# Performance work log

Hardware: AMD Instinct MI355X
Metric: run time of the kernel (lower is better)

Reference implementation:

```python
import jax, jax.numpy as jnp
import numpy as np

N_NODES = 50000
N_EDGES = 262144
N_OCP = 32768
N_GRAPHS = 64
H = 128          # hidden_size
F_IN = 128       # node feature dim (== H for the stub GNN)
N_LABELS = 10


def _lin(key, fan_in, fan_out):
    return jax.random.normal(key, (fan_in, fan_out), jnp.float32) * (1.0 / float(np.sqrt(fan_in)))


def setup_inputs() -> dict:
    key = jax.random.key(0)
    ks = jax.random.split(key, 16)
    x = jax.random.normal(ks[0], (N_NODES, F_IN), jnp.float32)
    edge_index = jax.random.randint(ks[1], (2, N_EDGES), 0, N_NODES)
    batch_vec = jnp.sort(jax.random.randint(ks[2], (N_NODES,), 0, N_GRAPHS))
    y = jax.random.randint(ks[3], (N_GRAPHS,), 0, N_LABELS)
    params = {
        # stub GNN (get_node_reps): one GCN-style layer
        'W_self': _lin(ks[4], F_IN, H),
        'W_nbr': _lin(ks[5], F_IN, H),
        'b_gnn': jnp.zeros((H,), jnp.float32),
        # edge_action_rep_generator: Linear(2H,4H) ELU Linear(4H,2H) ELU Linear(2H,H)
        'Wr1': _lin(ks[6], 2 * H, 4 * H), 'br1': jnp.zeros((4 * H,), jnp.float32),
        'Wr2': _lin(ks[7], 4 * H, 2 * H), 'br2': jnp.zeros((2 * H,), jnp.float32),
        'Wr3': _lin(ks[8], 2 * H, H),     'br3': jnp.zeros((H,), jnp.float32),
        # edge_action_prob_generator: Linear(H,H) ELU Linear(H,num_labels)
        'Wp1': _lin(ks[9], H, H),         'bp1': jnp.zeros((H,), jnp.float32),
        'Wp2': _lin(ks[10], H, N_LABELS), 'bp2': jnp.zeros((N_LABELS,), jnp.float32),
    }
    return dict(x=x, edge_index=edge_index, batch_vec=batch_vec, y=y, n_ocp=N_OCP, **params)


def reference(x, edge_index, batch_vec, y, n_ocp,
              W_self, W_nbr, b_gnn,
              Wr1, br1, Wr2, br2, Wr3, br3,
              Wp1, bp1, Wp2, bp2):
    N = x.shape[0]
    G = y.shape[0]

    def get_node_reps(ei):
        # stub for self.model.get_node_reps: elu(x @ W_self + A @ (x @ W_nbr))
        msg = x[ei[0]] @ W_nbr                                   # [E', H]
        agg = jax.ops.segment_sum(msg, ei[1], num_segments=N)    # [N, H]
        return jax.nn.elu(x @ W_self + agg + b_gnn)

    ocp_edge_index = edge_index[:, :n_ocp]    # state == True edges
    ava_edge_index = edge_index[:, n_ocp:]    # state == False edges

    ava_node_reps = get_node_reps(edge_index) - get_node_reps(ocp_edge_index)  # [N, H]

    # gather per available edge + concat src/dst reps -> [E_ava, 2H]
    a = jnp.concatenate([ava_node_reps[ava_edge_index[0]],
                         ava_node_reps[ava_edge_index[1]]], axis=1)
    # edge_action_rep_generator
    a = jax.nn.elu(a @ Wr1 + br1)
    a = jax.nn.elu(a @ Wr2 + br2)
    a = a @ Wr3 + br3                                            # [E_ava, H]
    # edge_action_prob_generator
    h = jax.nn.elu(a @ Wp1 + bp1)
    logits = h @ Wp2 + bp2                                       # [E_ava, L]

    seg = batch_vec[ava_edge_index[0]]                           # graph id per ava edge
    y_edge = y[seg]                                              # target label per edge
    sel = jnp.take_along_axis(logits, y_edge[:, None], axis=1)[:, 0]  # gather(1, y)

    # segment-wise softmax over edges of each graph
    mx = jax.ops.segment_max(sel, seg, num_segments=G)
    ex = jnp.exp(sel - mx[seg])
    probs = ex / jax.ops.segment_sum(ex, seg, num_segments=G)[seg]    # [E_ava]

    # scatter_max: per-graph max prob and its argmax edge index
    pmax = jax.ops.segment_max(probs, seg, num_segments=G)            # [G]
    E = probs.shape[0]
    idx = jnp.where(probs == pmax[seg], jnp.arange(E), E)
    added_actions = jax.ops.segment_min(idx, seg, num_segments=G)     # [G]

    return probs, pmax, added_actions
```

## Files before the change

kernel.cpp:

```cpp
#include <hip/hip_runtime.h>

#define NN   50000
#define NNP  50048
#define NE   262144
#define NOCP 32768
#define EAVA (NE - NOCP)
#define NG   64
#define HD   128
#define CAP  48
#define CHNK 32768

typedef _Float16 f16x8 __attribute__((ext_vector_type(8)));
typedef _Float16 f16x2 __attribute__((ext_vector_type(2)));
typedef float f32x4 __attribute__((ext_vector_type(4)));

#define WAITVM12() asm volatile("s_waitcnt vmcnt(12)" ::: "memory")
#define WAITVM6()  asm volatile("s_waitcnt vmcnt(6)" ::: "memory")
#define WAITVM0()  asm volatile("s_waitcnt vmcnt(0)" ::: "memory")

__device__ __forceinline__ float elu_f(float v) { return v > 0.f ? v : (expf(v) - 1.f); }

__device__ __forceinline__ unsigned fenc(float f) {
  unsigned u = __float_as_uint(f);
  return (u & 0x80000000u) ? ~u : (u | 0x80000000u);
}
__device__ __forceinline__ float fdec(unsigned u) {
  return __uint_as_float((u & 0x80000000u) ? (u & 0x7fffffffu) : ~u);
}

__device__ __forceinline__ void dma16(const void* g, void* l) {
  __builtin_amdgcn_global_load_lds((const __attribute__((address_space(1))) unsigned int*)g,
                                   (__attribute__((address_space(3))) unsigned int*)l,
                                   16, 0, 0);
}

__global__ __launch_bounds__(256) void zero_i(int* __restrict__ p, int n) {
  for (int i = blockIdx.x * 256 + threadIdx.x; i < n; i += gridDim.x * 256) p[i] = 0;
}

__global__ void init_small(unsigned* mx_enc, float* denom, unsigned* pmax_enc, int* amin) {
  int t = threadIdx.x;
  if (t < NG) { mx_enc[t] = 0u; denom[t] = 0.f; pmax_enc[t] = 0u; amin[t] = EAVA; }
}

__global__ __launch_bounds__(256) void zero_tails(_Float16* __restrict__ base) {
  int t = blockIdx.x * 256 + threadIdx.x;
  if (t >= 6 * 768) return;
  int arr = t / 768, off = t % 768;
  f16x8 z = {};
  *(f16x8*)(base + (size_t)arr * NNP * HD + (size_t)NN * HD + (size_t)off * 8) = z;
}

__global__ __launch_bounds__(256) void bucket_kernel(const int* __restrict__ ei,
    int* __restrict__ cnt, int* __restrict__ bucket) {
  int e = blockIdx.x * 256 + threadIdx.x;
  if (e >= NE) return;
  int dst = ei[NE + e];
  int src = ei[e];
  int slot = atomicAdd(&cnt[dst], 1);
  if (slot < CAP)
    bucket[(size_t)dst * CAP + slot] = (int)((unsigned)src | (e < NOCP ? 0x80000000u : 0u));
}

__global__ __launch_bounds__(256) void gather_kernel(const float* __restrict__ x,
    const int* __restrict__ cnt, const int* __restrict__ bucket,
    _Float16* __restrict__ xsah, _Float16* __restrict__ xsal,
    _Float16* __restrict__ xsoh, _Float16* __restrict__ xsol) {
  int n = blockIdx.x * 4 + (threadIdx.x >> 6);
  if (n >= NN) return;
  int lane = threadIdx.x & 63;
  int c = cnt[n];
  if (c > CAP) c = CAP;
  float2 aall = make_float2(0.f, 0.f), aocp = aall;
  const int* bk = bucket + (size_t)n * CAP;
  for (int i0 = 0; i0 < c; i0 += 4) {
    int4 pk = *(const int4*)(bk + i0);
    bool m1 = (i0 + 1 < c), m2 = (i0 + 2 < c), m3 = (i0 + 3 < c);
    int r0 = pk.x & 0x7fffffff;
    int r1 = m1 ? (pk.y & 0x7fffffff) : 0;
    int r2 = m2 ? (pk.z & 0x7fffffff) : 0;
    int r3 = m3 ? (pk.w & 0x7fffffff) : 0;
    float2 v0 = *(const float2*)(x + (size_t)r0 * HD + lane * 2);
    float2 v1 = *(const float2*)(x + (size_t)r1 * HD + lane * 2);
    float2 v2 = *(const float2*)(x + (size_t)r2 * HD + lane * 2);
    float2 v3 = *(const float2*)(x + (size_t)r3 * HD + lane * 2);
    aall.x += v0.x; aall.y += v0.y;
    if (pk.x < 0) { aocp.x += v0.x; aocp.y += v0.y; }
    if (m1) { aall.x += v1.x; aall.y += v1.y; if (pk.y < 0) { aocp.x += v1.x; aocp.y += v1.y; } }
    if (m2) { aall.x += v2.x; aall.y += v2.y; if (pk.z < 0) { aocp.x += v2.x; aocp.y += v2.y; } }
    if (m3) { aall.x += v3.x; aall.y += v3.y; if (pk.w < 0) { aocp.x += v3.x; aocp.y += v3.y; } }
  }
  size_t o = (size_t)n * HD + lane * 2;
  _Float16 h0 = (_Float16)aall.x, h1 = (_Float16)aall.y;
  *(f16x2*)(xsah + o) = (f16x2){h0, h1};
  *(f16x2*)(xsal + o) = (f16x2){(_Float16)(aall.x - (float)h0), (_Float16)(aall.y - (float)h1)};
  _Float16 g0 = (_Float16)aocp.x, g1 = (_Float16)aocp.y;
  *(f16x2*)(xsoh + o) = (f16x2){g0, g1};
  *(f16x2*)(xsol + o) = (f16x2){(_Float16)(aocp.x - (float)g0), (_Float16)(aocp.y - (float)g1)};
}

__global__ __launch_bounds__(256) void split_x(const float* __restrict__ r,
    _Float16* __restrict__ rh, _Float16* __restrict__ rl) {
  int t = blockIdx.x * 256 + threadIdx.x;
  if (t >= NN * HD / 8) return;
  const float4* p = (const float4*)(r + (size_t)t * 8);
  float4 v0 = p[0], v1 = p[1];
  float vv[8] = {v0.x, v0.y, v0.z, v0.w, v1.x, v1.y, v1.z, v1.w};
  f16x8 hv, lv;
#pragma unroll
  for (int j = 0; j < 8; ++j) {
    _Float16 hh = (_Float16)vv[j];
    hv[j] = hh;
    lv[j] = (_Float16)(vv[j] - (float)hh);
  }
  *(f16x8*)(rh + (size_t)t * 8) = hv;
  *(f16x8*)(rl + (size_t)t * 8) = lv;
}

__global__ void pack_w2(const float* __restrict__ Wself, const float* __restrict__ Wnbr,
    _Float16* __restrict__ oh, _Float16* __restrict__ ol) {
  int chunk = blockIdx.x;
  int lane = threadIdx.x;
  int ns = chunk & 7, kt = chunk >> 3;
  int n = ns * 16 + (lane & 15);
  int k0 = kt * 32 + (lane >> 4) * 8;
  f16x8 hv, lv;
#pragma unroll
  for (int j = 0; j < 8; ++j) {
    int k = k0 + j;
    float v = (k < 128) ? Wself[(size_t)k * 128 + n] : Wnbr[(size_t)(k - 128) * 128 + n];
    _Float16 hh = (_Float16)v;
    hv[j] = hh;
    lv[j] = (_Float16)(v - (float)hh);
  }
  *(f16x8*)(oh + (size_t)chunk * 512 + lane * 8) = hv;
  *(f16x8*)(ol + (size_t)chunk * 512 + lane * 8) = lv;
}

__global__ void pack_w(const float* __restrict__ W, int K, int N,
    _Float16* __restrict__ oh, _Float16* __restrict__ ol) {
  int chunk = blockIdx.x;
  int lane = threadIdx.x;
  int NS = N >> 4;
  int ns = chunk % NS, kt = chunk / NS;
  int n = ns * 16 + (lane & 15);
  int k0 = kt * 32 + (lane >> 4) * 8;
  f16x8 hv, lv;
#pragma unroll
  for (int j = 0; j < 8; ++j) {
    float v = W[(size_t)(k0 + j) * N + n];
    _Float16 hh = (_Float16)v;
    hv[j] = hh;
    lv[j] = (_Float16)(v - (float)hh);
  }
  *(f16x8*)(oh + (size_t)chunk * 512 + lane * 8) = hv;
  *(f16x8*)(ol + (size_t)chunk * 512 + lane * 8) = lv;
}

__global__ void w34_kernel(const float* __restrict__ Wr3, const float* __restrict__ Wp1,
    const float* __restrict__ br3, const float* __restrict__ bp1,
    float* __restrict__ W34, float* __restrict__ b34) {
  int i = blockIdx.x, j = threadIdx.x;
  float s = 0.f;
  for (int k = 0; k < 128; ++k) s += Wr3[i * 128 + k] * Wp1[k * 128 + j];
  W34[i * 128 + j] = s;
  if (i == 0) {
    float t = bp1[j];
    for (int k = 0; k < 128; ++k) t += br3[k] * Wp1[k * 128 + j];
    b34[j] = t;
  }
}

template <int KT, int NS_B, int AMODE, int KT_NEXT, int NB>
__global__ __launch_bounds__(256) void gemm_ab(
    const _Float16* __restrict__ Ah, const _Float16* __restrict__ Al,
    const int* __restrict__ idx0, const int* __restrict__ idx1,
    const _Float16* __restrict__ Bh, const _Float16* __restrict__ Bl,
    const float* __restrict__ bias,
    _Float16* __restrict__ Oh, _Float16* __restrict__ Ol) {
  __shared__ char smem[73728] __attribute__((aligned(16)));
  float* sC = (float*)smem;

  const int tid = threadIdx.x;
  const int w = tid >> 6, lane = tid & 63;
  const int l16 = lane & 15, g16 = lane >> 4;
  const int f = blockIdx.x;
  const int r8 = f & 7;
  const int nb = (f >> 3) % NB;
  const int q8 = f / (8 * NB);
  const int bm = (q8 * 8 + r8) * 128, bn = nb * 64;
  const int w2r = w >> 1, w2c = w & 1;
  const int bmT = bm >> 4, bnS = bn >> 4;

  f32x4 acc[4][2];
#pragma unroll
  for (int i = 0; i < 4; ++i)
#pragma unroll
    for (int j = 0; j < 2; ++j) acc[i][j] = (f32x4)0.f;

  int i0a = 0, i0b = 0, i1a = 0, i1b = 0;
  if constexpr (AMODE == 1) {
    int rr0 = bm + w * 32 + l16;
    i0a = idx0[rr0]; i0b = idx0[rr0 + 16];
    i1a = idx1[rr0]; i1b = idx1[rr0 + 16];
  }

  auto STAGE = [&](int kt, int buf) {
    char* base = smem + buf * 24576;
    if constexpr (AMODE == 0) {
#pragma unroll
      for (int s = 0; s < 2; ++s) {
        int msub = w * 2 + s;
        size_t ch = (size_t)(bmT + msub) * KT + kt;
        dma16((const char*)Ah + ch * 1024 + lane * 16, base + msub * 1024);
        dma16((const char*)Al + ch * 1024 + lane * 16, base + 8192 + msub * 1024);
      }
    } else {
      int col = (kt & 3) * 32 + g16 * 8;
      int r0 = (kt < 4) ? i0a : i1a;
      int r1 = (kt < 4) ? i0b : i1b;
      dma16(Ah + (size_t)r0 * HD + col, base + (w * 2) * 1024);
      dma16(Al + (size_t)r0 * HD + col, base + 8192 + (w * 2) * 1024);
      dma16(Ah + (size_t)r1 * HD + col, base + (w * 2 + 1) * 1024);
      dma16(Al + (size_t)r1 * HD + col, base + 8192 + (w * 2 + 1) * 1024);
    }
    size_t chb = (size_t)kt * NS_B + bnS + w;
    dma16((const char*)Bh + chb * 1024 + lane * 16, base + 16384 + w * 1024);
    dma16((const char*)Bl + chb * 1024 + lane * 16, base + 20480 + w * 1024);
  };

  auto COMPUTE = [&](int buf) {
    const _Float16* sAh = (const _Float16*)(smem + buf * 24576);
    const _Float16* sAl = (const _Float16*)(smem + buf * 24576 + 8192);
    const _Float16* sBh = (const _Float16*)(smem + buf * 24576 + 16384);
    const _Float16* sBl = (const _Float16*)(smem + buf * 24576 + 20480);
    f16x8 ah[4], al[4];
#pragma unroll
    for (int mi = 0; mi < 4; ++mi) {
      ah[mi] = *(const f16x8*)(sAh + (w2r * 4 + mi) * 512 + lane * 8);
      al[mi] = *(const f16x8*)(sAl + (w2r * 4 + mi) * 512 + lane * 8);
    }
#pragma unroll
    for (int ni = 0; ni < 2; ++ni) {
      f16x8 bh = *(const f16x8*)(sBh + (w2c * 2 + ni) * 512 + lane * 8);
      f16x8 bl = *(const f16x8*)(sBl + (w2c * 2 + ni) * 512 + lane * 8);
#pragma unroll
      for (int mi = 0; mi < 4; ++mi) {
        acc[mi][ni] = __builtin_amdgcn_mfma_f32_16x16x32_f16(ah[mi], bh, acc[mi][ni], 0, 0, 0);
        acc[mi][ni] = __builtin_amdgcn_mfma_f32_16x16x32_f16(al[mi], bh, acc[mi][ni], 0, 0, 0);
        acc[mi][ni] = __builtin_amdgcn_mfma_f32_16x16x32_f16(ah[mi], bl, acc[mi][ni], 0, 0, 0);
      }
    }
  };

  STAGE(0, 0);
  STAGE(1, 1);
#pragma unroll
  for (int kt = 0; kt < KT; ++kt) {
    if (kt + 2 < KT) STAGE(kt + 2, (kt + 2) % 3);
    if (kt < KT - 2) WAITVM12();
    else if (kt == KT - 2) WAITVM6();
    else WAITVM0();
    __builtin_amdgcn_s_barrier();
    COMPUTE(kt % 3);
    __builtin_amdgcn_s_barrier();
  }

#pragma unroll
  for (int ni = 0; ni < 2; ++ni) {
    int colL = (w2c * 2 + ni) * 16 + l16;
    float bv = bias[bn + colL];
#pragma unroll
    for (int mi = 0; mi < 4; ++mi) {
      int rowb = w2r * 64 + mi * 16 + g16 * 4;
#pragma unroll
      for (int r = 0; r < 4; ++r)
        sC[(rowb + r) * 68 + colL] = elu_f(acc[mi][ni][r] + bv);
    }
  }
  __syncthreads();
  const int bnT32 = bn >> 5;
#pragma unroll
  for (int c = 0; c < 4; ++c) {
    int chunkid = w * 4 + c;
    int msub = chunkid >> 1, ktl = chunkid & 1;
    int m = msub * 16 + l16;
    int cb = ktl * 32 + g16 * 8;
    f16x8 hv, lv;
#pragma unroll
    for (int j = 0; j < 8; ++j) {
      float v = sC[m * 68 + cb + j];
      _Float16 hh = (_Float16)v;
      hv[j] = hh;
      lv[j] = (_Float16)(v - (float)hh);
    }
    size_t gchunk = (size_t)(bmT + msub) * KT_NEXT + (bnT32 + ktl);
    *(f16x8*)((char*)Oh + gchunk * 1024 + lane * 16) = hv;
    *(f16x8*)((char*)Ol + gchunk * 1024 + lane * 16) = lv;
  }
}

__global__ __launch_bounds__(64) void reps_direct(
    const _Float16* __restrict__ xh, const _Float16* __restrict__ xl,
    const _Float16* __restrict__ xsah, const _Float16* __restrict__ xsal,
    const _Float16* __restrict__ xsoh, const _Float16* __restrict__ xsol,
    const _Float16* __restrict__ Wsh, const _Float16* __restrict__ Wsl,
    const float* __restrict__ bias,
    _Float16* __restrict__ Oh, _Float16* __restrict__ Ol) {
  __shared__ float sC[32][68];
  const int lane = threadIdx.x;
  const int mt = blockIdx.x, nt = blockIdx.y;
  const int bm = mt * 32, bn = nt * 64;
  const int l16 = lane & 15, g16 = lane >> 4;

  f32x4 acc1[2][4], acc2[2][4];
#pragma unroll
  for (int i = 0; i < 2; ++i)
#pragma unroll
    for (int j = 0; j < 4; ++j) acc1[i][j] = (f32x4)0.f;

  auto CP3 = [&](f32x4 (*acc)[4], const f16x8* ah, const f16x8* al,
                 const f16x8* bh, const f16x8* bl) {
#pragma unroll
    for (int ni = 0; ni < 4; ++ni)
#pragma unroll
      for (int mi = 0; mi < 2; ++mi) {
        acc[mi][ni] = __builtin_amdgcn_mfma_f32_16x16x32_f16(ah[mi], bh[ni], acc[mi][ni], 0, 0, 0);
        acc[mi][ni] = __builtin_amdgcn_mfma_f32_16x16x32_f16(al[mi], bh[ni], acc[mi][ni], 0, 0, 0);
        acc[mi][ni] = __builtin_amdgcn_mfma_f32_16x16x32_f16(ah[mi], bl[ni], acc[mi][ni], 0, 0, 0);
      }
  };

#pragma unroll
  for (int kt = 0; kt < 4; ++kt) {
    f16x8 ah[2], al[2], bh[4], bl[4];
#pragma unroll
    for (int mi = 0; mi < 2; ++mi) {
      size_t off = (size_t)(bm + mi * 16 + l16) * HD + kt * 32 + g16 * 8;
      ah[mi] = *(const f16x8*)(xh + off);
      al[mi] = *(const f16x8*)(xl + off);
    }
#pragma unroll
    for (int ni = 0; ni < 4; ++ni) {
      size_t ch = (size_t)kt * 8 + nt * 4 + ni;
      bh[ni] = *(const f16x8*)(Wsh + ch * 512 + lane * 8);
      bl[ni] = *(const f16x8*)(Wsl + ch * 512 + lane * 8);
    }
    CP3(acc1, ah, al, bh, bl);
  }
#pragma unroll
  for (int i = 0; i < 2; ++i)
#pragma unroll
    for (int j = 0; j < 4; ++j) acc2[i][j] = acc1[i][j];

#pragma unroll
  for (int kt = 0; kt < 4; ++kt) {
    f16x8 aah[2], aal[2], aoh[2], aol[2], bh[4], bl[4];
#pragma unroll
    for (int mi = 0; mi < 2; ++mi) {
      size_t off = (size_t)(bm + mi * 16 + l16) * HD + kt * 32 + g16 * 8;
      aah[mi] = *(const f16x8*)(xsah + off);
      aal[mi] = *(const f16x8*)(xsal + off);
      aoh[mi] = *(const f16x8*)(xsoh + off);
      aol[mi] = *(const f16x8*)(xsol + off);
    }
#pragma unroll
    for (int ni = 0; ni < 4; ++ni) {
      size_t ch = (size_t)(kt + 4) * 8 + nt * 4 + ni;
      bh[ni] = *(const f16x8*)(Wsh + ch * 512 + lane * 8);
      bl[ni] = *(const f16x8*)(Wsl + ch * 512 + lane * 8);
    }
    CP3(acc1, aah, aal, bh, bl);
    CP3(acc2, aoh, aol, bh, bl);
  }

#pragma unroll
  for (int ni = 0; ni < 4; ++ni) {
    int colL = ni * 16 + l16;
    float bv = bias[bn + colL];
#pragma unroll
    for (int mi = 0; mi < 2; ++mi) {
      int rowb = mi * 16 + g16 * 4;
#pragma unroll
      for (int r = 0; r < 4; ++r)
        sC[rowb + r][colL] = elu_f(acc1[mi][ni][r] + bv) - elu_f(acc2[mi][ni][r] + bv);
    }
  }
  __syncthreads();
#pragma unroll
  for (int c = 0; c < 4; ++c) {
    int msub = c >> 1, ktl = c & 1;
    int m = msub * 16 + l16;
    int cb = ktl * 32 + g16 * 8;
    int grow = bm + m;
    if (grow < NN) {
      f16x8 hv, lv;
#pragma unroll
      for (int j = 0; j < 8; ++j) {
        float v = sC[m][cb + j];
        _Float16 hh = (_Float16)v;
        hv[j] = hh;
        lv[j] = (_Float16)(v - (float)hh);
      }
      *(f16x8*)(Oh + (size_t)grow * HD + bn + cb) = hv;
      *(f16x8*)(Ol + (size_t)grow * HD + bn + cb) = lv;
    }
  }
}

__global__ __launch_bounds__(256) void gemm3_sel(
    const _Float16* __restrict__ Ah, const _Float16* __restrict__ Al,
    const _Float16* __restrict__ Bh, const _Float16* __restrict__ Bl,
    const float* __restrict__ b34,
    const int* __restrict__ ei, const int* __restrict__ batchv, const int* __restrict__ yv,
    const float* __restrict__ Wp2, const float* __restrict__ bp2,
    float* __restrict__ sel, int* __restrict__ seg, int co) {
  __shared__ char smem[73728] __attribute__((aligned(16)));
  const int tid = threadIdx.x;
  const int w = tid >> 6, lane = tid & 63;
  const int l16 = lane & 15, g16 = lane >> 4;
  const int mt = blockIdx.x;

  f32x4 acc[8];
#pragma unroll
  for (int j = 0; j < 8; ++j) acc[j] = (f32x4)0.f;

  auto STAGE = [&](int kt, int buf) {
    char* base = smem + buf * 24576;
    size_t ch = (size_t)(mt * 4 + w) * 8 + kt;
    dma16((const char*)Ah + ch * 1024 + lane * 16, base + w * 1024);
    dma16((const char*)Al + ch * 1024 + lane * 16, base + 4096 + w * 1024);
#pragma unroll
    for (int s = 0; s < 2; ++s) {
      int nsub = w * 2 + s;
      size_t chb = (size_t)kt * 8 + nsub;
      dma16((const char*)Bh + chb * 1024 + lane * 16, base + 8192 + nsub * 1024);
      dma16((const char*)Bl + chb * 1024 + lane * 16, base + 16384 + nsub * 1024);
    }
  };

  auto COMPUTE = [&](int buf) {
    const _Float16* sAh = (const _Float16*)(smem + buf * 24576);
    const _Float16* sAl = (const _Float16*)(smem + buf * 24576 + 4096);
    const _Float16* sBh = (const _Float16*)(smem + buf * 24576 + 8192);
    const _Float16* sBl = (const _Float16*)(smem + buf * 24576 + 16384);
    f16x8 ah = *(const f16x8*)(sAh + w * 512 + lane * 8);
    f16x8 al = *(const f16x8*)(sAl + w * 512 + lane * 8);
#pragma unroll
    for (int ni = 0; ni < 8; ++ni) {
      f16x8 bh = *(const f16x8*)(sBh + ni * 512 + lane * 8);
      f16x8 bl = *(const f16x8*)(sBl + ni * 512 + lane * 8);
      acc[ni] = __builtin_amdgcn_mfma_f32_16x16x32_f16(ah, bh, acc[ni], 0, 0, 0);
      acc[ni] = __builtin_amdgcn_mfma_f32_16x16x32_f16(al, bh, acc[ni], 0, 0, 0);
      acc[ni] = __builtin_amdgcn_mfma_f32_16x16x32_f16(ah, bl, acc[ni], 0, 0, 0);
    }
  };

  STAGE(0, 0);
  STAGE(1, 1);
#pragma unroll
  for (int kt = 0; kt < 8; ++kt) {
    if (kt + 2 < 8) STAGE(kt + 2, (kt + 2) % 3);
    if (kt < 6) WAITVM12();
    else if (kt == 6) WAITVM6();
    else WAITVM0();
    __builtin_amdgcn_s_barrier();
    COMPUTE(kt % 3);
    __builtin_amdgcn_s_barrier();
  }

  float bb[8];
#pragma unroll
  for (int ni = 0; ni < 8; ++ni) bb[ni] = b34[ni * 16 + l16];

#pragma unroll
  for (int rr = 0; rr < 4; ++rr) {
    int row = w * 16 + g16 * 4 + rr;
    int e = co + mt * 64 + row;
    int s = ei[NOCP + e];
    int gg = batchv[s];
    int c = yv[gg];
    float a = 0.f;
#pragma unroll
    for (int ni = 0; ni < 8; ++ni)
      a += elu_f(acc[ni][rr] + bb[ni]) * Wp2[(ni * 16 + l16) * 10 + c];
    a += __shfl_xor(a, 1);
    a += __shfl_xor(a, 2);
    a += __shfl_xor(a, 4);
    a += __shfl_xor(a, 8);
    if (l16 == 0) { sel[e] = a + bp2[c]; seg[e] = gg; }
  }
}

__global__ __launch_bounds__(256) void segmax_sel(const float* __restrict__ sel,
    const int* __restrict__ seg, unsigned* __restrict__ mx_enc) {
  __shared__ unsigned sm[NG];
  int tid = threadIdx.x;
  if (tid < NG) sm[tid] = 0u;
  __syncthreads();
  for (int i = blockIdx.x * blockDim.x + tid; i < EAVA; i += gridDim.x * blockDim.x)
    atomicMax(&sm[seg[i]], fenc(sel[i]));
  __syncthreads();
  if (tid < NG) atomicMax(&mx_enc[tid], sm[tid]);
}

__global__ __launch_bounds__(256) void exden_kernel(const float* __restrict__ sel,
    const int* __restrict__ seg, const unsigned* __restrict__ mx_enc,
    float* __restrict__ denom, float* __restrict__ out_probs) {
  __shared__ float sd[NG];
  __shared__ float smx[NG];
  int tid = threadIdx.x;
  if (tid < NG) { smx[tid] = fdec(mx_enc[tid]); sd[tid] = 0.f; }
  __syncthreads();
  for (int i = blockIdx.x * blockDim.x + tid; i < EAVA; i += gridDim.x * blockDim.x) {
    int g = seg[i];
    float ex = expf(sel[i] - smx[g]);
    out_probs[i] = ex;
    atomicAdd(&sd[g], ex);
  }
  __syncthreads();
  if (tid < NG) atomicAdd(&denom[tid], sd[tid]);
}

__global__ __launch_bounds__(256) void probpmax_kernel(const int* __restrict__ seg,
    const float* __restrict__ denom, float* __restrict__ out_probs,
    unsigned* __restrict__ pmax_enc) {
  __shared__ float sden[NG];
  __shared__ unsigned sp[NG];
  int tid = threadIdx.x;
  if (tid < NG) { sden[tid] = denom[tid]; sp[tid] = 0u; }
  __syncthreads();
  for (int i = blockIdx.x * blockDim.x + tid; i < EAVA; i += gridDim.x * blockDim.x) {
    int g = seg[i];
    float p = out_probs[i] / sden[g];
    out_probs[i] = p;
    atomicMax(&sp[g], fenc(p));
  }
  __syncthreads();
  if (tid < NG) atomicMax(&pmax_enc[tid], sp[tid]);
}

__global__ __launch_bounds__(256) void argmin_kernel(const int* __restrict__ seg,
    const float* __restrict__ out_probs, const unsigned* __restrict__ pmax_enc,
    int* __restrict__ amin) {
  __shared__ float spm[NG];
  __shared__ int sa[NG];
  int tid = threadIdx.x;
  if (tid < NG) { spm[tid] = fdec(pmax_enc[tid]); sa[tid] = EAVA; }
  __syncthreads();
  for (int i = blockIdx.x * blockDim.x + tid; i < EAVA; i += gridDim.x * blockDim.x) {
    int g = seg[i];
    if (out_probs[i] == spm[g]) atomicMin(&sa[g], i);
  }
  __syncthreads();
  if (tid < NG) atomicMin(&amin[tid], sa[tid]);
}

__global__ void finalize_kernel(const unsigned* __restrict__ pmax_enc,
    const int* __restrict__ amin, float* __restrict__ out) {
  int g = threadIdx.x;
  if (g < NG) {
    out[EAVA + g] = fdec(pmax_enc[g]);
    out[EAVA + NG + g] = (float)amin[g];
  }
}

extern "C" void kernel_launch(void* const* d_in, const int* in_sizes, int n_in,
                              void* d_out, int out_size, void* d_ws, size_t ws_size,
                              hipStream_t stream) {
  const float* x      = (const float*)d_in[0];
  const int*   ei     = (const int*)d_in[1];
  const int*   batchv = (const int*)d_in[2];
  const int*   yv     = (const int*)d_in[3];
  const float* Wself = (const float*)d_in[5];
  const float* Wnbr  = (const float*)d_in[6];
  const float* bgnn  = (const float*)d_in[7];
  const float* Wr1   = (const float*)d_in[8];
  const float* br1   = (const float*)d_in[9];
  const float* Wr2   = (const float*)d_in[10];
  const float* br2   = (const float*)d_in[11];
  const float* Wr3   = (const float*)d_in[12];
  const float* br3   = (const float*)d_in[13];
  const float* Wp1   = (const float*)d_in[14];
  const float* bp1   = (const float*)d_in[15];
  const float* Wp2   = (const float*)d_in[16];
  const float* bp2   = (const float*)d_in[17];
  float* out = (float*)d_out;

  char* wp = (char*)d_ws;
  auto alloc = [&](size_t bytes) -> char* {
    char* p = wp;
    wp += (bytes + 255) & ~(size_t)255;
    return p;
  };
  _Float16* xsplit = (_Float16*)alloc((size_t)6 * NNP * HD * 2);
  _Float16* xh   = xsplit + (size_t)0 * NNP * HD;
  _Float16* xl   = xsplit + (size_t)1 * NNP * HD;
  _Float16* xsah = xsplit + (size_t)2 * NNP * HD;
  _Float16* xsal = xsplit + (size_t)3 * NNP * HD;
  _Float16* xsoh = xsplit + (size_t)4 * NNP * HD;
  _Float16* xsol = xsplit + (size_t)5 * NNP * HD;
  _Float16*  reps_h   = (_Float16*)alloc((size_t)NN * HD * 2);
  _Float16*  reps_l   = (_Float16*)alloc((size_t)NN * HD * 2);
  int*       cnt      = (int*)alloc((size_t)NN * 4);
  int*       bucket   = (int*)alloc((size_t)NN * CAP * 4);
  float*     sel      = (float*)alloc((size_t)EAVA * 4);
  int*       seg      = (int*)alloc((size_t)EAVA * 4);
  unsigned*  mx_enc   = (unsigned*)alloc(NG * 4);
  float*     denom    = (float*)alloc(NG * 4);
  unsigned*  pmax_enc = (unsigned*)alloc(NG * 4);
  int*       amin     = (int*)alloc(NG * 4);
  _Float16*  Wsh  = (_Float16*)alloc((size_t)64 * 1024);
  _Float16*  Wsl  = (_Float16*)alloc((size_t)64 * 1024);
  _Float16*  Wr1h = (_Float16*)alloc((size_t)8 * 32 * 1024);
  _Float16*  Wr1l = (_Float16*)alloc((size_t)8 * 32 * 1024);
  _Float16*  Wr2h = (_Float16*)alloc((size_t)16 * 16 * 1024);
  _Float16*  Wr2l = (_Float16*)alloc((size_t)16 * 16 * 1024);
  float*     W34  = (float*)alloc((size_t)256 * 128 * 4);
  float*     b34  = (float*)alloc(128 * 4);
  _Float16*  W34h = (_Float16*)alloc((size_t)8 * 8 * 1024);
  _Float16*  W34l = (_Float16*)alloc((size_t)8 * 8 * 1024);

  const size_t b1_full = (size_t)(EAVA / 16) * 16 * 1024;
  const size_t b2_full = (size_t)(EAVA / 16) * 8 * 1024;
  size_t used = (size_t)(wp - (char*)d_ws);
  bool full = ws_size >= used + 2 * b1_full + 2 * b2_full + (1u << 20);

  _Float16 *b1h, *b1l, *b2h, *b2l;
  if (full) {
    b1h = (_Float16*)alloc(b1_full);
    b1l = (_Float16*)alloc(b1_full);
    b2h = (_Float16*)alloc(b2_full);
    b2l = (_Float16*)alloc(b2_full);
  } else {
    b1h = (_Float16*)alloc((size_t)(CHNK / 16) * 16 * 1024);
    b1l = (_Float16*)alloc((size_t)(CHNK / 16) * 16 * 1024);
    b2h = (_Float16*)alloc((size_t)(CHNK / 16) * 8 * 1024);
    b2l = (_Float16*)alloc((size_t)(CHNK / 16) * 8 * 1024);
  }
  (void)ws_size;

  zero_i<<<64, 256, 0, stream>>>(cnt, NN);
  init_small<<<1, 64, 0, stream>>>(mx_enc, denom, pmax_enc, amin);
  zero_tails<<<18, 256, 0, stream>>>(xsplit);
  bucket_kernel<<<NE / 256, 256, 0, stream>>>(ei, cnt, bucket);
  gather_kernel<<<(NN + 3) / 4, 256, 0, stream>>>(x, cnt, bucket, xsah, xsal, xsoh, xsol);
  split_x<<<(NN * HD / 8 + 255) / 256, 256, 0, stream>>>(x, xh, xl);
  pack_w2<<<64, 64, 0, stream>>>(Wself, Wnbr, Wsh, Wsl);
  reps_direct<<<dim3(NNP / 32, 2), 64, 0, stream>>>(xh, xl, xsah, xsal, xsoh, xsol, Wsh, Wsl,
                                                    bgnn, reps_h, reps_l);
  w34_kernel<<<256, 128, 0, stream>>>(Wr3, Wp1, br3, bp1, W34, b34);
  pack_w<<<8 * 32, 64, 0, stream>>>(Wr1, 256, 512, Wr1h, Wr1l);
  pack_w<<<16 * 16, 64, 0, stream>>>(Wr2, 512, 256, Wr2h, Wr2l);
  pack_w<<<8 * 8, 64, 0, stream>>>(W34, 256, 128, W34h, W34l);

  if (full) {
    gemm_ab<8, 32, 1, 16, 8><<<(EAVA / 128) * 8, 256, 0, stream>>>(
        reps_h, reps_l, ei + NOCP, ei + NE + NOCP, Wr1h, Wr1l, br1, b1h, b1l);
    gemm_ab<16, 16, 0, 8, 4><<<(EAVA / 128) * 4, 256, 0, stream>>>(
        b1h, b1l, nullptr, nullptr, Wr2h, Wr2l, br2, b2h, b2l);
    gemm3_sel<<<EAVA / 64, 256, 0, stream>>>(
        b2h, b2l, W34h, W34l, b34, ei, batchv, yv, Wp2, bp2, sel, seg, 0);
  } else {
    for (int c = 0; c < 7; ++c) {
      int co = c * CHNK;
      gemm_ab<8, 32, 1, 16, 8><<<(CHNK / 128) * 8, 256, 0, stream>>>(
          reps_h, reps_l, ei + NOCP + co, ei + NE + NOCP + co, Wr1h, Wr1l, br1, b1h, b1l);
      gemm_ab<16, 16, 0, 8, 4><<<(CHNK / 128) * 4, 256, 0, stream>>>(
          b1h, b1l, nullptr, nullptr, Wr2h, Wr2l, br2, b2h, b2l);
      gemm3_sel<<<CHNK / 64, 256, 0, stream>>>(
          b2h, b2l, W34h, W34l, b34, ei, batchv, yv, Wp2, bp2, sel, seg, co);
    }
  }

  segmax_sel<<<112, 256, 0, stream>>>(sel, seg, mx_enc);
  exden_kernel<<<112, 256, 0, stream>>>(sel, seg, mx_enc, denom, out);
  probpmax_kernel<<<112, 256, 0, stream>>>(seg, denom, out, pmax_enc);
  argmin_kernel<<<112, 256, 0, stream>>>(seg, out, pmax_enc, amin);
  finalize_kernel<<<1, 64, 0, stream>>>(pmax_enc, amin, out);
}
```

Measured before the change: 907.0 us.

## Precompute per-node first-layer projections and gather them per edge

The first MLP layer on concatenated endpoint reps is split algebraically into node-level products P=reps@Wr1[:128] and Q=reps@Wr1[128:]. These are computed once over ~50k nodes instead of over ~229k edges. A new fuse kernel then gathers P[src]+Q[dst]+bias, applies ELU, and writes the split-f16 tiles for layer 2. This removes most of the layer-1 FLOPs, at the cost of a large fp32 PQ buffer (~200MB) and the random gather traffic that goes with it. The previous full-buffer path is dropped, so layers 2 and 3 now always run in 7 chunks.

Result: slower. 926.7 us (+2.2%).

```diff
diff --git a/kernel.cpp b/kernel.cpp
--- a/kernel.cpp
+++ b/kernel.cpp
@@ -2,6 +2,7 @@
 
 #define NN   50000
 #define NNP  50048
+#define NNP2 50176
 #define NE   262144
 #define NOCP 32768
 #define EAVA (NE - NOCP)
@@ -157,6 +158,43 @@
   *(f16x8*)(ol + (size_t)chunk * 512 + lane * 8) = lv;
 }
 
+__global__ void pack_w1cat(const float* __restrict__ Wr1,
+    _Float16* __restrict__ oh, _Float16* __restrict__ ol) {
+  int chunk = blockIdx.x;
+  int lane = threadIdx.x;
+  int ns = chunk & 63, kt = chunk >> 6;
+  int n = ns * 16 + (lane & 15);
+  int k0 = kt * 32 + (lane >> 4) * 8;
+  f16x8 hv, lv;
+#pragma unroll
+  for (int j = 0; j < 8; ++j) {
+    int k = k0 + j;
+    float v = (n < 512) ? Wr1[(size_t)k * 512 + n] : Wr1[(size_t)(128 + k) * 512 + (n - 512)];
+    _Float16 hh = (_Float16)v;
+    hv[j] = hh;
+    lv[j] = (_Float16)(v - (float)hh);
+  }
+  *(f16x8*)(oh + (size_t)chunk * 512 + lane * 8) = hv;
+  *(f16x8*)(ol + (size_t)chunk * 512 + lane * 8) = lv;
+}
+
+__global__ __launch_bounds__(256) void pack_acts(const _Float16* __restrict__ rh,
+    const _Float16* __restrict__ rl, _Float16* __restrict__ oh, _Float16* __restrict__ ol) {
+  int tid = threadIdx.x;
+  int w = tid >> 6, lane = tid & 63;
+  int chunkid = blockIdx.x * 4 + w;
+  int rt = chunkid >> 2, ktl = chunkid & 3;
+  int grow = rt * 16 + (lane & 15);
+  f16x8 hv = {}, lv = {};
+  if (grow < NN) {
+    size_t off = (size_t)grow * HD + ktl * 32 + (lane >> 4) * 8;
+    hv = *(const f16x8*)(rh + off);
+    lv = *(const f16x8*)(rl + off);
+  }
+  *(f16x8*)(oh + (size_t)chunkid * 512 + lane * 8) = hv;
+  *(f16x8*)(ol + (size_t)chunkid * 512 + lane * 8) = lv;
+}
+
 __global__ void w34_kernel(const float* __restrict__ Wr3, const float* __restrict__ Wp1,
     const float* __restrict__ br3, const float* __restrict__ bp1,
     float* __restrict__ W34, float* __restrict__ b34) {
@@ -171,13 +209,14 @@
   }
 }
 
-template <int KT, int NS_B, int AMODE, int KT_NEXT, int NB>
+template <int KT, int NS_B, int AMODE, int KT_NEXT, int NB, int OMODE = 0>
 __global__ __launch_bounds__(256) void gemm_ab(
     const _Float16* __restrict__ Ah, const _Float16* __restrict__ Al,
     const int* __restrict__ idx0, const int* __restrict__ idx1,
     const _Float16* __restrict__ Bh, const _Float16* __restrict__ Bl,
     const float* __restrict__ bias,
-    _Float16* __restrict__ Oh, _Float16* __restrict__ Ol) {
+    _Float16* __restrict__ Oh, _Float16* __restrict__ Ol,
+    float* __restrict__ Orows) {
   __shared__ char smem[73728] __attribute__((aligned(16)));
   float* sC = (float*)smem;
 
@@ -266,37 +305,101 @@
     __builtin_amdgcn_s_barrier();
   }
 
-#pragma unroll
-  for (int ni = 0; ni < 2; ++ni) {
-    int colL = (w2c * 2 + ni) * 16 + l16;
-    float bv = bias[bn + colL];
-#pragma unroll
-    for (int mi = 0; mi < 4; ++mi) {
-      int rowb = w2r * 64 + mi * 16 + g16 * 4;
-#pragma unroll
-      for (int r = 0; r < 4; ++r)
-        sC[(rowb + r) * 68 + colL] = elu_f(acc[mi][ni][r] + bv);
-    }
-  }
-  __syncthreads();
-  const int bnT32 = bn >> 5;
-#pragma unroll
-  for (int c = 0; c < 4; ++c) {
-    int chunkid = w * 4 + c;
-    int msub = chunkid >> 1, ktl = chunkid & 1;
-    int m = msub * 16 + l16;
-    int cb = ktl * 32 + g16 * 8;
+  if constexpr (OMODE == 1) {
+    const int ON = NS_B * 16;
+#pragma unroll
+    for (int ni = 0; ni < 2; ++ni) {
+      int colg = bn + (w2c * 2 + ni) * 16 + l16;
+#pragma unroll
+      for (int mi = 0; mi < 4; ++mi) {
+        int rowb = bm + w2r * 64 + mi * 16 + g16 * 4;
+#pragma unroll
+        for (int r = 0; r < 4; ++r)
+          Orows[(size_t)(rowb + r) * ON + colg] = acc[mi][ni][r];
+      }
+    }
+  } else {
+#pragma unroll
+    for (int ni = 0; ni < 2; ++ni) {
+      int colL = (w2c * 2 + ni) * 16 + l16;
+      float bv = bias[bn + colL];
+#pragma unroll
+      for (int mi = 0; mi < 4; ++mi) {
+        int rowb = w2r * 64 + mi * 16 + g16 * 4;
+#pragma unroll
+        for (int r = 0; r < 4; ++r)
+          sC[(rowb + r) * 68 + colL] = elu_f(acc[mi][ni][r] + bv);
+      }
+    }
+    __syncthreads();
+    const int bnT32 = bn >> 5;
+#pragma unroll
+    for (int c = 0; c < 4; ++c) {
+      int chunkid = w * 4 + c;
+      int msub = chunkid >> 1, ktl = chunkid & 1;
+      int m = msub * 16 + l16;
+      int cb = ktl * 32 + g16 * 8;
+      f16x8 hv, lv;
+#pragma unroll
+      for (int j = 0; j < 8; ++j) {
+        float v = sC[m * 68 + cb + j];
+        _Float16 hh = (_Float16)v;
+        hv[j] = hh;
+        lv[j] = (_Float16)(v - (float)hh);
+      }
+      size_t gchunk = (size_t)(bmT + msub) * KT_NEXT + (bnT32 + ktl);
+      *(f16x8*)((char*)Oh + gchunk * 1024 + lane * 16) = hv;
+      *(f16x8*)((char*)Ol + gchunk * 1024 + lane * 16) = lv;
+    }
+  }
+}
+
+__global__ __launch_bounds__(256) void l1_fuse(
+    const float* __restrict__ PQ, const float* __restrict__ br1,
+    const int* __restrict__ ei,
+    _Float16* __restrict__ b1h, _Float16* __restrict__ b1l, int co) {
+  __shared__ _Float16 sh[16][520];
+  __shared__ _Float16 sl[16][520];
+  const int tid = threadIdx.x;
+  const int w = tid >> 6, lane = tid & 63;
+  const int l16 = lane & 15, g16 = lane >> 4;
+
+#pragma unroll
+  for (int t = 0; t < 4; ++t) {
+    int el = w * 4 + t;
+    int e = co + blockIdx.x * 16 + el;
+    int i0 = ei[NOCP + e];
+    int i1 = ei[NE + NOCP + e];
+    const float* p = PQ + (size_t)i0 * 1024;
+    const float* q = PQ + (size_t)i1 * 1024 + 512;
+    float4 pa = *(const float4*)(p + lane * 8);
+    float4 pb = *(const float4*)(p + lane * 8 + 4);
+    float4 qa = *(const float4*)(q + lane * 8);
+    float4 qb = *(const float4*)(q + lane * 8 + 4);
+    float4 ba = *(const float4*)(br1 + lane * 8);
+    float4 bb = *(const float4*)(br1 + lane * 8 + 4);
+    float s[8] = {pa.x + qa.x + ba.x, pa.y + qa.y + ba.y, pa.z + qa.z + ba.z, pa.w + qa.w + ba.w,
+                  pb.x + qb.x + bb.x, pb.y + qb.y + bb.y, pb.z + qb.z + bb.z, pb.w + qb.w + bb.w};
     f16x8 hv, lv;
 #pragma unroll
     for (int j = 0; j < 8; ++j) {
-      float v = sC[m * 68 + cb + j];
+      float v = elu_f(s[j]);
       _Float16 hh = (_Float16)v;
       hv[j] = hh;
       lv[j] = (_Float16)(v - (float)hh);
     }
-    size_t gchunk = (size_t)(bmT + msub) * KT_NEXT + (bnT32 + ktl);
-    *(f16x8*)((char*)Oh + gchunk * 1024 + lane * 16) = hv;
-    *(f16x8*)((char*)Ol + gchunk * 1024 + lane * 16) = lv;
+    *(f16x8*)&sh[el][lane * 8] = hv;
+    *(f16x8*)&sl[el][lane * 8] = lv;
+  }
+  __syncthreads();
+#pragma unroll
+  for (int it = 0; it < 4; ++it) {
+    int kt = w * 4 + it;
+    f16x8 hv = *(const f16x8*)&sh[l16][kt * 32 + g16 * 8];
+    f16x8 lv = *(const f16x8*)&sl[l16][kt * 32 + g16 * 8];
+    size_t gchunk = (size_t)blockIdx.x * 16 + kt;
+    *(f16x8*)(b1h + gchunk * 512 + lane * 8) = hv;
+    *(f16x8*)(b1l + gchunk * 512 + lane * 8) = lv;
   }
 }
 
@@ -620,23 +723,25 @@
   float*     b34  = (float*)alloc(128 * 4);
   _Float16*  W34h = (_Float16*)alloc((size_t)8 * 8 * 1024);
   _Float16*  W34l = (_Float16*)alloc((size_t)8 * 8 * 1024);
-
-  const size_t b1_full = (size_t)(EAVA / 16) * 16 * 1024;
-  const size_t b2_full = (size_t)(EAVA / 16) * 8 * 1024;
+  _Float16*  b1h = (_Float16*)alloc((size_t)(CHNK / 16) * 16 * 1024);
+  _Float16*  b1l = (_Float16*)alloc((size_t)(CHNK / 16) * 16 * 1024);
+  _Float16*  b2h = (_Float16*)alloc((size_t)(CHNK / 16) * 8 * 1024);
+  _Float16*  b2l = (_Float16*)alloc((size_t)(CHNK / 16) * 8 * 1024);
+
+  const size_t pq_bytes   = (size_t)NNP2 * 1024 * 4;
+  const size_t apq_bytes  = (size_t)(NNP2 / 16) * 4 * 1024;
+  const size_t w1c_bytes  = (size_t)256 * 1024;
   size_t used = (size_t)(wp - (char*)d_ws);
-  bool full = ws_size >= used + 2 * b1_full + 2 * b2_full + (1u << 20);
-
-  _Float16 *b1h, *b1l, *b2h, *b2l;
-  if (full) {
-    b1h = (_Float16*)alloc(b1_full);
-    b1l = (_Float16*)alloc(b1_full);
-    b2h = (_Float16*)alloc(b2_full);
-    b2l = (_Float16*)alloc(b2_full);
-  } else {
-    b1h = (_Float16*)alloc((size_t)(CHNK / 16) * 16 * 1024);
-    b1l = (_Float16*)alloc((size_t)(CHNK / 16) * 16 * 1024);
-    b2h = (_Float16*)alloc((size_t)(CHNK / 16) * 8 * 1024);
-    b2l = (_Float16*)alloc((size_t)(CHNK / 16) * 8 * 1024);
+  bool pq_ok = ws_size >= used + pq_bytes + 2 * apq_bytes + 2 * w1c_bytes + (1u << 20);
+
+  float* PQ = nullptr;
+  _Float16 *Apqh = nullptr, *Apql = nullptr, *W1ch = nullptr, *W1cl = nullptr;
+  if (pq_ok) {
+    PQ   = (float*)alloc(pq_bytes);
+    Apqh = (_Float16*)alloc(apq_bytes);
+    Apql = (_Float16*)alloc(apq_bytes);
+    W1ch = (_Float16*)alloc(w1c_bytes);
+    W1cl = (_Float16*)alloc(w1c_bytes);
   }
   (void)ws_size;
 
@@ -650,24 +755,31 @@
   reps_direct<<<dim3(NNP / 32, 2), 64, 0, stream>>>(xh, xl, xsah, xsal, xsoh, xsol, Wsh, Wsl,
                                                     bgnn, reps_h, reps_l);
   w34_kernel<<<256, 128, 0, stream>>>(Wr3, Wp1, br3, bp1, W34, b34);
-  pack_w<<<8 * 32, 64, 0, stream>>>(Wr1, 256, 512, Wr1h, Wr1l);
   pack_w<<<16 * 16, 64, 0, stream>>>(Wr2, 512, 256, Wr2h, Wr2l);
   pack_w<<<8 * 8, 64, 0, stream>>>(W34, 256, 128, W34h, W34l);
 
-  if (full) {
-    gemm_ab<8, 32, 1, 16, 8><<<(EAVA / 128) * 8, 256, 0, stream>>>(
-        reps_h, reps_l, ei + NOCP, ei + NE + NOCP, Wr1h, Wr1l, br1, b1h, b1l);
-    gemm_ab<16, 16, 0, 8, 4><<<(EAVA / 128) * 4, 256, 0, stream>>>(
-        b1h, b1l, nullptr, nullptr, Wr2h, Wr2l, br2, b2h, b2l);
-    gemm3_sel<<<EAVA / 64, 256, 0, stream>>>(
-        b2h, b2l, W34h, W34l, b34, ei, batchv, yv, Wp2, bp2, sel, seg, 0);
+  if (pq_ok) {
+    pack_w1cat<<<256, 64, 0, stream>>>(Wr1, W1ch, W1cl);
+    pack_acts<<<NNP2 / 64, 256, 0, stream>>>(reps_h, reps_l, Apqh, Apql);
+    gemm_ab<4, 64, 0, 0, 16, 1><<<(NNP2 / 128) * 16, 256, 0, stream>>>(
+        Apqh, Apql, nullptr, nullptr, W1ch, W1cl, nullptr, nullptr, nullptr, PQ);
+    for (int c = 0; c < 7; ++c) {
+      int co = c * CHNK;
+      l1_fuse<<<CHNK / 16, 256, 0, stream>>>(PQ, br1, ei, b1h, b1l, co);
+      gemm_ab<16, 16, 0, 8, 4><<<(CHNK / 128) * 4, 256, 0, stream>>>(
+          b1h, b1l, nullptr, nullptr, Wr2h, Wr2l, br2, b2h, b2l, nullptr);
+      gemm3_sel<<<CHNK / 64, 256, 0, stream>>>(
+          b2h, b2l, W34h, W34l, b34, ei, batchv, yv, Wp2, bp2, sel, seg, co);
+    }
   } else {
+    pack_w<<<8 * 32, 64, 0, stream>>>(Wr1, 256, 512, Wr1h, Wr1l);
     for (int c = 0; c < 7; ++c) {
       int co = c * CHNK;
       gemm_ab<8, 32, 1, 16, 8><<<(CHNK / 128) * 8, 256, 0, stream>>>(
-          reps_h, reps_l, ei + NOCP + co, ei + NE + NOCP + co, Wr1h, Wr1l, br1, b1h, b1l);
+          reps_h, reps_l, ei + NOCP + co, ei + NE + NOCP + co, Wr1h, Wr1l, br1, b1h, b1l,
+          nullptr);
       gemm_ab<16, 16, 0, 8, 4><<<(CHNK / 128) * 4, 256, 0, stream>>>(
-          b1h, b1l, nullptr, nullptr, Wr2h, Wr2l, br2, b2h, b2l);
+          b1h, b1l, nullptr, nullptr, Wr2h, Wr2l, br2, b2h, b2l, nullptr);
       gemm3_sel<<<CHNK / 64, 256, 0, stream>>>(
           b2h, b2l, W34h, W34l, b34, ei, batchv, yv, Wp2, bp2, sel, seg, co);
     }
```
